# Kernel optimization log

Hardware: AMD Instinct MI355X
Metric: run time of the kernel (lower is better)

Reference implementation:

```python
import jax, jax.numpy as jnp
import numpy as np

B, L, D, H, F, NL, K, G = 2, 2048, 768, 12, 3072, 12, 128, 16
HD = D // H
SCALE = HD ** -0.5


def setup_inputs() -> dict:
    key = jax.random.key(0)
    ks = jax.random.split(key, 8)
    n = lambda k, s, std=0.02: jax.random.normal(k, s, dtype=jnp.float32) * std
    return {
        "x": jax.random.normal(ks[0], (B, L, D), dtype=jnp.float32),
        "pos_conv_w": n(ks[1], (D, D // G, K)),
        "pos_conv_b": jnp.zeros((D,), jnp.float32),
        "ln0_g": jnp.ones((D,), jnp.float32), "ln0_b": jnp.zeros((D,), jnp.float32),
        "Wq": n(ks[2], (NL, D, D)), "bq": jnp.zeros((NL, D), jnp.float32),
        "Wk": n(ks[3], (NL, D, D)), "bk": jnp.zeros((NL, D), jnp.float32),
        "Wv": n(ks[4], (NL, D, D)), "bv": jnp.zeros((NL, D), jnp.float32),
        "Wo": n(ks[5], (NL, D, D)), "bo": jnp.zeros((NL, D), jnp.float32),
        "ln1_g": jnp.ones((NL, D), jnp.float32), "ln1_b": jnp.zeros((NL, D), jnp.float32),
        "W1": n(ks[6], (NL, D, F)), "b1": jnp.zeros((NL, F), jnp.float32),
        "W2": n(ks[7], (NL, F, D)), "b2": jnp.zeros((NL, D), jnp.float32),
        "ln2_g": jnp.ones((NL, D), jnp.float32), "ln2_b": jnp.zeros((NL, D), jnp.float32),
    }


def _ln(x, g, b, eps=1e-5):
    m = jnp.mean(x, axis=-1, keepdims=True)
    v = jnp.mean(jnp.square(x - m), axis=-1, keepdims=True)
    return (x - m) * jax.lax.rsqrt(v + eps) * g + b


def reference(x, pos_conv_w, pos_conv_b, ln0_g, ln0_b, Wq, bq, Wk, bk, Wv, bv, Wo, bo,
              ln1_g, ln1_b, W1, b1, W2, b2, ln2_g, ln2_b):
    b_, l_, d_ = x.shape
    # positional grouped conv embedding (kernel even -> drop last frame), GELU, residual add
    pos = jax.lax.conv_general_dilated(x.transpose(0, 2, 1), pos_conv_w, (1,), [(K // 2, K // 2)],
                                       feature_group_count=G)  # (B, D, L+1)
    pos = pos[:, :, :l_] + pos_conv_b[None, :, None]
    h = x + jax.nn.gelu(pos, approximate=False).transpose(0, 2, 1)
    # post-norm encoder (layer_norm_first=False): LN applied before the layer stack
    h = _ln(h, ln0_g, ln0_b)

    def layer(h, p):
        wq, bq_, wk, bk_, wv, bv_, wo, bo_, g1, be1, w1, bf1, w2, bf2, g2, be2 = p
        r = h
        q = (h @ wq + bq_).reshape(b_, l_, H, HD)
        k = (h @ wk + bk_).reshape(b_, l_, H, HD)
        v = (h @ wv + bv_).reshape(b_, l_, H, HD)
        w = jax.nn.softmax(SCALE * jnp.einsum('blhd,bmhd->bhlm', q, k), axis=-1)
        o = jnp.einsum('bhlm,bmhd->blhd', w, v).reshape(b_, l_, d_)
        h = r + (o @ wo + bo_)
        h = _ln(h, g1, be1)
        ff = jax.nn.gelu(h @ w1 + bf1, approximate=False) @ w2 + bf2
        h = _ln(h + ff, g2, be2)
        return h, None

    h, _ = jax.lax.scan(layer, h, (Wq, bq, Wk, bk, Wv, bv, Wo, bo,
                                   ln1_g, ln1_b, W1, b1, W2, b2, ln2_g, ln2_b))
    return h
```

## Files before the change

kernel.cpp:

```cpp
#include <hip/hip_runtime.h>
#include <hip/hip_bf16.h>
#include <stdint.h>

#define B_ 2
#define L_ 2048
#define D_ 768
#define H_ 12
#define F_ 3072
#define NL_ 12
#define K_ 128
#define G_ 16
#define HD_ 64
#define CPG_ 48
#define M_TOK (B_*L_)
#define SCALE_ 0.125f

typedef __hip_bfloat16 bf16;
typedef __bf16 bf16x8 __attribute__((ext_vector_type(8)));
typedef float f32x4 __attribute__((ext_vector_type(4)));

__device__ __forceinline__ void gload16(const void* g, void* l) {
  __builtin_amdgcn_global_load_lds((const __attribute__((address_space(1))) void*)g,
                                   (__attribute__((address_space(3))) void*)l, 16, 0, 0);
}

__global__ __launch_bounds__(256) void convw_kernel(const float* __restrict__ w,
                                                    bf16* __restrict__ wT2) {
  int idx = blockIdx.x * 256 + threadIdx.x;
  int ci = idx & 63;
  int row = idx >> 6;
  int d = row % 48;
  int t2 = row / 48;
  int kk = t2 & 127;
  int g = t2 >> 7;
  float v = (ci < 48) ? w[(((size_t)(g * 48 + d) * 48) + ci) * 128 + kk] : 0.f;
  wT2[idx] = __float2bfloat16(v);
}

__global__ __launch_bounds__(256) void conv_mfma(const float* __restrict__ x,
                                                 const bf16* __restrict__ wT2,
                                                 const float* __restrict__ bias,
                                                 float* __restrict__ out) {
  const int l0 = blockIdx.x * 64, g = blockIdx.y, b = blockIdx.z;
  const int tid = threadIdx.x, w = tid >> 6, lane = tid & 63;
  const int c15 = lane & 15, g4 = lane >> 4;
  __shared__ __align__(16) bf16 win[192 * 72];
  __shared__ __align__(16) bf16 Wl[2 * 48 * 64];

  if (tid < 192) {
    int lg = l0 - 64 + tid;
    char* dst = (char*)win + tid * 144;
    uint4 z4 = {0u, 0u, 0u, 0u};
    if ((unsigned)lg < 2048u) {
      const float* srow = x + ((size_t)(b * 2048 + lg) * 768 + g * 48);
#pragma unroll
      for (int c = 0; c < 6; ++c) {
        float4 v0 = *(const float4*)(srow + c * 8);
        float4 v1 = *(const float4*)(srow + c * 8 + 4);
        union { bf16 h[8]; uint4 u; } uu;
        uu.h[0] = __float2bfloat16(v0.x); uu.h[1] = __float2bfloat16(v0.y);
        uu.h[2] = __float2bfloat16(v0.z); uu.h[3] = __float2bfloat16(v0.w);
        uu.h[4] = __float2bfloat16(v1.x); uu.h[5] = __float2bfloat16(v1.y);
        uu.h[6] = __float2bfloat16(v1.z); uu.h[7] = __float2bfloat16(v1.w);
        *(uint4*)(dst + c * 16) = uu.u;
      }
    } else {
#pragma unroll
      for (int c = 0; c < 6; ++c) *(uint4*)(dst + c * 16) = z4;
    }
    *(uint4*)(dst + 96) = z4;
    *(uint4*)(dst + 112) = z4;
  }
  __syncthreads();

  f32x4 acc[3];
  const f32x4 vzero = {0.f, 0.f, 0.f, 0.f};
  acc[0] = vzero; acc[1] = vzero; acc[2] = vzero;

  const char* wbase = (const char*)wT2 + (size_t)g * 128 * 48 * 128;

  for (int kp = 0; kp < 64; ++kp) {
#pragma unroll
    for (int i = 0; i < 3; ++i) {
      int coff = w * 3072 + i * 1024;
      int c = coff + (lane << 4);
      int row96 = c >> 7;
      int s = row96 / 48;
      int d = row96 - s * 48;
      int cb2 = c & 127;
      gload16(wbase + ((size_t)((2 * kp + s) * 48 + d)) * 128 + (cb2 ^ ((d & 7) << 4)),
              (char*)Wl + coff);
    }
    __syncthreads();
#pragma unroll
    for (int s = 0; s < 2; ++s) {
      int kk = 2 * kp + s;
#pragma unroll
      for (int cb = 0; cb < 2; ++cb) {
        bf16x8 a = *(const bf16x8*)((const char*)win + (w * 16 + c15 + kk) * 144 + cb * 64 + g4 * 16);
#pragma unroll
        for (int ct = 0; ct < 3; ++ct) {
          int d = ct * 16 + c15;
          bf16x8 bfrag = *(const bf16x8*)((const char*)Wl + s * 6144 + d * 128 +
                                          ((cb * 64 + g4 * 16) ^ ((d & 7) << 4)));
          acc[ct] = __builtin_amdgcn_mfma_f32_16x16x32_bf16(a, bfrag, acc[ct], 0, 0, 0);
        }
      }
    }
    __syncthreads();
  }

#pragma unroll
  for (int ct = 0; ct < 3; ++ct) {
    int dg = g * 48 + ct * 16 + c15;
    float bv = bias[dg];
#pragma unroll
    for (int r = 0; r < 4; ++r) {
      int l = l0 + w * 16 + g4 * 4 + r;
      size_t idx = (size_t)(b * 2048 + l) * 768 + dg;
      float vv = acc[ct][r] + bv;
      vv = 0.5f * vv * (1.0f + erff(vv * 0.70710678f));
      out[idx] = x[idx] + vv;
    }
  }
}

__global__ __launch_bounds__(256) void ln_kernel(const float* __restrict__ a,
                                                 const float* __restrict__ r,
                                                 const float* __restrict__ g,
                                                 const float* __restrict__ be,
                                                 float* __restrict__ out,
                                                 bf16* __restrict__ outb) {
  int w = threadIdx.x >> 6, lane = threadIdx.x & 63;
  size_t row = (size_t)blockIdx.x * 4 + w;
  const float* ar = a + row * 768;
  const float* rr = r ? r + row * 768 : nullptr;
  float4 v[3];
  float s = 0.f;
#pragma unroll
  for (int i = 0; i < 3; ++i) {
    int c = lane * 4 + i * 256;
    float4 vv = *(const float4*)(ar + c);
    if (rr) {
      float4 rv = *(const float4*)(rr + c);
      vv.x += rv.x; vv.y += rv.y; vv.z += rv.z; vv.w += rv.w;
    }
    v[i] = vv;
    s += vv.x + vv.y + vv.z + vv.w;
  }
#pragma unroll
  for (int st = 1; st < 64; st <<= 1) s += __shfl_xor(s, st);
  float mean = s * (1.0f / 768.0f);
  float s2 = 0.f;
#pragma unroll
  for (int i = 0; i < 3; ++i) {
    float dx = v[i].x - mean, dy = v[i].y - mean, dz = v[i].z - mean, dw = v[i].w - mean;
    s2 += dx * dx + dy * dy + dz * dz + dw * dw;
  }
#pragma unroll
  for (int st = 1; st < 64; st <<= 1) s2 += __shfl_xor(s2, st);
  float rstd = rsqrtf(s2 * (1.0f / 768.0f) + 1e-5f);
#pragma unroll
  for (int i = 0; i < 3; ++i) {
    int c = lane * 4 + i * 256;
    float4 gv = *(const float4*)(g + c);
    float4 bv = *(const float4*)(be + c);
    float4 ov;
    ov.x = (v[i].x - mean) * rstd * gv.x + bv.x;
    ov.y = (v[i].y - mean) * rstd * gv.y + bv.y;
    ov.z = (v[i].z - mean) * rstd * gv.z + bv.z;
    ov.w = (v[i].w - mean) * rstd * gv.w + bv.w;
    *(float4*)(out + row * 768 + c) = ov;
    if (outb) {
      union { bf16 h[4]; uint2 u; } pk;
      pk.h[0] = __float2bfloat16(ov.x); pk.h[1] = __float2bfloat16(ov.y);
      pk.h[2] = __float2bfloat16(ov.z); pk.h[3] = __float2bfloat16(ov.w);
      *(uint2*)(outb + row * 768 + c) = pk.u;
    }
  }
}

__global__ __launch_bounds__(256) void castT_kernel(const float* __restrict__ src,
                                                    bf16* __restrict__ dst, int R, int C) {
  __shared__ float t[32][33];
  int c0 = blockIdx.x * 32, r0 = blockIdx.y * 32;
  int tx = threadIdx.x & 31, ty = threadIdx.x >> 5;
#pragma unroll
  for (int i = 0; i < 32; i += 8)
    t[ty + i][tx] = src[(size_t)(r0 + ty + i) * C + (c0 + tx)];
  __syncthreads();
#pragma unroll
  for (int i = 0; i < 32; i += 8)
    dst[(size_t)(c0 + ty + i) * R + (r0 + tx)] = __float2bfloat16(t[tx][ty + i]);
}

__global__ __launch_bounds__(256) void castT_qkv_kernel(const float* __restrict__ q,
                                                        const float* __restrict__ k,
                                                        const float* __restrict__ v,
                                                        bf16* __restrict__ dst) {
  int n0 = blockIdx.x * 32, k0 = blockIdx.y * 32;
  const float* src = (n0 < 768) ? q : (n0 < 1536) ? k : v;
  int nn = (n0 >= 1536) ? (n0 - 1536) : (n0 >= 768 ? n0 - 768 : n0);
  __shared__ float t[32][33];
  int tx = threadIdx.x & 31, ty = threadIdx.x >> 5;
#pragma unroll
  for (int i = 0; i < 32; i += 8)
    t[ty + i][tx] = src[(size_t)(k0 + ty + i) * 768 + nn + tx];
  __syncthreads();
#pragma unroll
  for (int i = 0; i < 32; i += 8)
    dst[(size_t)(n0 + ty + i) * 768 + k0 + tx] = __float2bfloat16(t[tx][ty + i]);
}

__global__ __launch_bounds__(256) void bcat_kernel(const float* __restrict__ bq,
                                                   const float* __restrict__ bk,
                                                   const float* __restrict__ bv,
                                                   float* __restrict__ dst) {
  int i = blockIdx.x * 256 + threadIdx.x;
  if (i >= 2304) return;
  dst[i] = (i < 768) ? bq[i] : (i < 1536) ? bk[i - 768] : bv[i - 1536];
}

__global__ __launch_bounds__(256) void vtrans_kernel(const bf16* __restrict__ qkv,
                                                     bf16* __restrict__ vT) {
  int l0 = blockIdx.x * 32, d0 = blockIdx.y * 32, bh = blockIdx.z;
  int b = bh / 12, h = bh % 12;
  __shared__ bf16 t[32][33];
  int tx = threadIdx.x & 31, ty = threadIdx.x >> 5;
#pragma unroll
  for (int i = 0; i < 32; i += 8)
    t[ty + i][tx] = qkv[(size_t)(b * 2048 + l0 + ty + i) * 2304 + 1536 + h * 64 + d0 + tx];
  __syncthreads();
#pragma unroll
  for (int i = 0; i < 32; i += 8)
    vT[((size_t)bh * 64 + d0 + ty + i) * 2048 + l0 + tx] = t[tx][ty + i];
}

template <int BM, int BN, int GELU, int BF16OUT>
__global__ __launch_bounds__(256) void gemm_bf16(const bf16* __restrict__ A,
                                                 const bf16* __restrict__ BT,
                                                 const float* __restrict__ bias,
                                                 void* __restrict__ Cout,
                                                 int N, int Kd) {
  constexpr int WM = BM / 2, MF = WM / 16;
  constexpr int WN = BN / 2, FN = WN / 16;
  __shared__ bf16 As[BM * 64];
  __shared__ bf16 Bs[BN * 64];
  const int tid = threadIdx.x, w = tid >> 6, lane = tid & 63;
  int gx = gridDim.x;
  int flat = blockIdx.x + gx * blockIdx.y;
  int cpx = (gx * gridDim.y) >> 3;
  int sw = (flat & 7) * cpx + (flat >> 3);
  const int bn = sw % gx, bm = sw / gx;
  const int wr = w >> 1, wc = w & 1;
  const int c15 = lane & 15, g4 = lane >> 4;
  const int lrow8 = lane >> 3;
  const int cb = (lane & 7) * 16;

  f32x4 acc[MF][FN];
  const f32x4 vzero = {0.f, 0.f, 0.f, 0.f};
#pragma unroll
  for (int i = 0; i < MF; ++i)
#pragma unroll
    for (int j = 0; j < FN; ++j) acc[i][j] = vzero;

  const char* Ab = (const char*)A;
  const char* Bb = (const char*)BT;

  for (int k0 = 0; k0 < Kd; k0 += 64) {
#pragma unroll
    for (int i = 0; i < BM / 32; ++i) {
      int t = w + 4 * i;
      int row = t * 8 + lrow8;
      gload16(Ab + ((size_t)(bm * BM + row) * Kd + k0) * 2 + (cb ^ ((row & 7) << 4)),
              (char*)As + t * 1024);
    }
#pragma unroll
    for (int i = 0; i < BN / 32; ++i) {
      int t = w + 4 * i;
      int row = t * 8 + lrow8;
      gload16(Bb + ((size_t)(bn * BN + row) * Kd + k0) * 2 + (cb ^ ((row & 7) << 4)),
              (char*)Bs + t * 1024);
    }
    __syncthreads();
    bf16x8 af[MF][2], bfr[FN][2];
#pragma unroll
    for (int kf = 0; kf < 2; ++kf) {
      int kbyte = kf * 64 + g4 * 16;
#pragma unroll
      for (int mf = 0; mf < MF; ++mf) {
        int row = wr * WM + mf * 16 + c15;
        af[mf][kf] = *(const bf16x8*)((const char*)As + row * 128 + (kbyte ^ ((row & 7) << 4)));
      }
#pragma unroll
      for (int fn = 0; fn < FN; ++fn) {
        int row = wc * WN + fn * 16 + c15;
        bfr[fn][kf] = *(const bf16x8*)((const char*)Bs + row * 128 + (kbyte ^ ((row & 7) << 4)));
      }
    }
    __builtin_amdgcn_s_setprio(1);
#pragma unroll
    for (int mf = 0; mf < MF; ++mf)
#pragma unroll
      for (int fn = 0; fn < FN; ++fn) {
        acc[mf][fn] = __builtin_amdgcn_mfma_f32_16x16x32_bf16(af[mf][0], bfr[fn][0], acc[mf][fn], 0, 0, 0);
        acc[mf][fn] = __builtin_amdgcn_mfma_f32_16x16x32_bf16(af[mf][1], bfr[fn][1], acc[mf][fn], 0, 0, 0);
      }
    __builtin_amdgcn_s_setprio(0);
    __syncthreads();
  }
#pragma unroll
  for (int fn = 0; fn < FN; ++fn) {
    int col = bn * BN + wc * WN + fn * 16 + c15;
    float bv = bias[col];
#pragma unroll
    for (int mf = 0; mf < MF; ++mf) {
#pragma unroll
      for (int r = 0; r < 4; ++r) {
        int row = bm * BM + wr * WM + mf * 16 + g4 * 4 + r;
        float vv = acc[mf][fn][r] + bv;
        if (GELU) vv = 0.5f * vv * (1.0f + erff(vv * 0.70710678f));
        if (BF16OUT) ((bf16*)Cout)[(size_t)row * N + col] = __float2bfloat16(vv);
        else        ((float*)Cout)[(size_t)row * N + col] = vv;
      }
    }
  }
}

__global__ __launch_bounds__(256) void attn_mfma(const bf16* __restrict__ qkv,
                                                 const bf16* __restrict__ vT,
                                                 bf16* __restrict__ ob) {
  int bid = blockIdx.x + 32 * (blockIdx.y + 12 * blockIdx.z);
  int wgid = (bid & 7) * 96 + (bid >> 3);
  const int q0 = (wgid & 31) * 64;
  int bh = wgid >> 5;
  const int h = bh % 12, b = bh / 12;

  const int tid = threadIdx.x, w = tid >> 6, lane = tid & 63;
  const int c15 = lane & 15, g4 = lane >> 4;
  const int lrow8 = lane >> 3;
  const int cb = (lane & 7) * 16;
  __shared__ bf16 Kl[2][4096];
  __shared__ bf16 Vl[2][4096];
  __shared__ bf16 Pl[4096];

  const f32x4 vzero = {0.f, 0.f, 0.f, 0.f};
  const char* qp = (const char*)qkv + (((size_t)(b * 2048 + q0 + w * 16 + c15)) * 2304 + h * 64) * 2;
  bf16x8 qa0 = *(const bf16x8*)(qp + g4 * 16);
  bf16x8 qa1 = *(const bf16x8*)(qp + 64 + g4 * 16);

  bf16x8 b_one;
#pragma unroll
  for (int i = 0; i < 8; ++i) b_one[i] = (__bf16)1.0f;

  f32x4 o[4], o5;
#pragma unroll
  for (int i = 0; i < 4; ++i) o[i] = vzero;
  o5 = vzero;
  float m = -1e30f;
  const float SC2 = 0.18033688f;
  const float THR = 11.54f;

  const char* kgb = (const char*)qkv + (((size_t)(b * 2048)) * 2304 + 768 + h * 64) * 2;
  const char* vgb = (const char*)vT + ((size_t)((b * 12 + h) * 64) * 2048) * 2;
  char* Plw = (char*)Pl + w * 2048;

#define STAGE(kt, bufi)                                                                     \
  {                                                                                         \
    char* Kd = (char*)Kl[bufi];                                                             \
    char* Vd = (char*)Vl[bufi];                                                             \
    _Pragma("unroll")                                                                       \
    for (int i = 0; i < 2; ++i) {                                                           \
      int t = w + 4 * i;                                                                    \
      int rr = t * 8 + lrow8;                                                               \
      gload16(kgb + (size_t)((kt) * 64 + rr) * 4608 + (cb ^ ((rr & 7) << 4)), Kd + t * 1024);\
      gload16(vgb + (size_t)rr * 4096 + (size_t)(kt) * 128 + (cb ^ ((rr & 7) << 4)), Vd + t * 1024);\
    }                                                                                       \
  }

  STAGE(0, 0);
  __syncthreads();

  for (int kt = 0; kt < 32; ++kt) {
    int cur = kt & 1;
    if (kt + 1 < 32) STAGE(kt + 1, cur ^ 1);

    const char* Kc = (const char*)Kl[cur];
    const char* Vc = (const char*)Vl[cur];

    f32x4 sc[4];
    __builtin_amdgcn_s_setprio(1);
#pragma unroll
    for (int fn = 0; fn < 4; ++fn) {
      int key = fn * 16 + c15;
      const char* kr = Kc + key * 128;
      int sw = (key & 7) << 4;
      bf16x8 kb0 = *(const bf16x8*)(kr + ((g4 * 16) ^ sw));
      bf16x8 kb1 = *(const bf16x8*)(kr + ((64 + g4 * 16) ^ sw));
      f32x4 s = __builtin_amdgcn_mfma_f32_16x16x32_bf16(kb0, qa0, vzero, 0, 0, 0);
      s = __builtin_amdgcn_mfma_f32_16x16x32_bf16(kb1, qa1, s, 0, 0, 0);
      sc[fn] = s;
    }
    __builtin_amdgcn_s_setprio(0);

    float pm = fmaxf(
        fmaxf(fmaxf(fmaxf(sc[0][0], sc[0][1]), fmaxf(sc[0][2], sc[0][3])),
              fmaxf(fmaxf(sc[1][0], sc[1][1]), fmaxf(sc[1][2], sc[1][3]))),
        fmaxf(fmaxf(fmaxf(sc[2][0], sc[2][1]), fmaxf(sc[2][2], sc[2][3])),
              fmaxf(fmaxf(sc[3][0], sc[3][1]), fmaxf(sc[3][2], sc[3][3]))));
    int ok = (pm * SC2 <= m + THR) ? 1 : 0;

    if (!__all(ok)) {
      float tm = pm;
      tm = fmaxf(tm, __shfl_xor(tm, 16));
      tm = fmaxf(tm, __shfl_xor(tm, 32));
      float mn = fmaxf(m, tm * SC2);
      float alpha = exp2f(m - mn);
      m = mn;
#pragma unroll
      for (int r = 0; r < 4; ++r) {
        float ar = __shfl(alpha, g4 * 4 + r);
        o[0][r] *= ar; o[1][r] *= ar; o[2][r] *= ar; o[3][r] *= ar;
        o5[r] *= ar;
      }
    }

    {
      char* prow = Plw + c15 * 128;
      int swp = (c15 & 7) << 4;
#pragma unroll
      for (int fn = 0; fn < 4; ++fn) {
        union { bf16 hh[4]; uint2 u; } pk;
#pragma unroll
        for (int r = 0; r < 4; ++r)
          pk.hh[r] = __float2bfloat16(exp2f(fmaf(sc[fn][r], SC2, -m)));
        *(uint2*)(prow + ((fn * 32 + g4 * 8) ^ swp)) = pk.u;
      }
    }

    {
      const char* pr = Plw + c15 * 128;
      int sw = (c15 & 7) << 4;
      bf16x8 pa0 = *(const bf16x8*)(pr + ((g4 * 16) ^ sw));
      bf16x8 pa1 = *(const bf16x8*)(pr + ((64 + g4 * 16) ^ sw));
      __builtin_amdgcn_s_setprio(1);
#pragma unroll
      for (int fh = 0; fh < 4; ++fh) {
        int hd = fh * 16 + c15;
        const char* vr = Vc + hd * 128;
        int swv = (hd & 7) << 4;
        bf16x8 vb0 = *(const bf16x8*)(vr + ((g4 * 16) ^ swv));
        bf16x8 vb1 = *(const bf16x8*)(vr + ((64 + g4 * 16) ^ swv));
        o[fh] = __builtin_amdgcn_mfma_f32_16x16x32_bf16(pa0, vb0, o[fh], 0, 0, 0);
        o[fh] = __builtin_amdgcn_mfma_f32_16x16x32_bf16(pa1, vb1, o[fh], 0, 0, 0);
      }
      o5 = __builtin_amdgcn_mfma_f32_16x16x32_bf16(pa0, b_one, o5, 0, 0, 0);
      o5 = __builtin_amdgcn_mfma_f32_16x16x32_bf16(pa1, b_one, o5, 0, 0, 0);
      __builtin_amdgcn_s_setprio(0);
    }
    __syncthreads();
  }
#undef STAGE

#pragma unroll
  for (int r = 0; r < 4; ++r) {
    float inv = 1.0f / o5[r];
    size_t row = (size_t)(b * 2048 + q0 + w * 16 + g4 * 4 + r);
#pragma unroll
    for (int fh = 0; fh < 4; ++fh)
      ob[row * 768 + h * 64 + fh * 16 + c15] = __float2bfloat16(o[fh][r] * inv);
  }
}

extern "C" void kernel_launch(void* const* d_in, const int* in_sizes, int n_in,
                              void* d_out, int out_size, void* d_ws, size_t ws_size,
                              hipStream_t stream) {
  const float* x      = (const float*)d_in[0];
  const float* pcw    = (const float*)d_in[1];
  const float* pcb    = (const float*)d_in[2];
  const float* ln0_g  = (const float*)d_in[3];
  const float* ln0_b  = (const float*)d_in[4];
  const float* Wq     = (const float*)d_in[5];
  const float* bq     = (const float*)d_in[6];
  const float* Wk     = (const float*)d_in[7];
  const float* bk     = (const float*)d_in[8];
  const float* Wv     = (const float*)d_in[9];
  const float* bv     = (const float*)d_in[10];
  const float* Wo     = (const float*)d_in[11];
  const float* bo     = (const float*)d_in[12];
  const float* ln1_g  = (const float*)d_in[13];
  const float* ln1_b  = (const float*)d_in[14];
  const float* W1     = (const float*)d_in[15];
  const float* b1     = (const float*)d_in[16];
  const float* W2     = (const float*)d_in[17];
  const float* b2     = (const float*)d_in[18];
  const float* ln2_g  = (const float*)d_in[19];
  const float* ln2_b  = (const float*)d_in[20];

  const size_t MDB = (size_t)M_TOK * D_ * 4;
  char* W = (char*)d_ws;
  float* h    = (float*)W;
  float* tmp  = (float*)(W + MDB);
  char*  big  = W + 2 * MDB;
  bf16*  qkv  = (bf16*)big;
  bf16*  ff   = (bf16*)big;
  bf16*  wT2  = (bf16*)big;
  char* p = W + 2 * MDB + 25165824;
  bf16* h_bf  = (bf16*)p; p += (size_t)M_TOK * D_ * 2;
  bf16* obuf  = (bf16*)p; p += (size_t)M_TOK * D_ * 2;
  bf16* vT    = (bf16*)p; p += (size_t)M_TOK * D_ * 2;
  bf16* wqkvb = (bf16*)p; p += (size_t)2304 * 768 * 2;
  bf16* wob   = (bf16*)p; p += (size_t)768 * 768 * 2;
  bf16* w1b   = (bf16*)p; p += (size_t)3072 * 768 * 2;
  bf16* w2b   = (bf16*)p; p += (size_t)768 * 3072 * 2;
  float* bqkv = (float*)p;

  convw_kernel<<<24576, 256, 0, stream>>>(pcw, wT2);
  conv_mfma<<<dim3(32, 16, 2), 256, 0, stream>>>(x, wT2, pcb, tmp);
  ln_kernel<<<M_TOK / 4, 256, 0, stream>>>(tmp, nullptr, ln0_g, ln0_b, h, h_bf);

  for (int l = 0; l < NL_; ++l) {
    const float* wq = Wq + (size_t)l * D_ * D_;
    const float* wk = Wk + (size_t)l * D_ * D_;
    const float* wv = Wv + (size_t)l * D_ * D_;
    const float* wo = Wo + (size_t)l * D_ * D_;
    const float* w1 = W1 + (size_t)l * D_ * F_;
    const float* w2 = W2 + (size_t)l * F_ * D_;

    castT_qkv_kernel<<<dim3(72, 24), 256, 0, stream>>>(wq, wk, wv, wqkvb);
    bcat_kernel<<<9, 256, 0, stream>>>(bq + (size_t)l * D_, bk + (size_t)l * D_, bv + (size_t)l * D_, bqkv);
    castT_kernel<<<dim3(24, 24), 256, 0, stream>>>(wo, wob, 768, 768);
    castT_kernel<<<dim3(96, 24), 256, 0, stream>>>(w1, w1b, 768, 3072);
    castT_kernel<<<dim3(24, 96), 256, 0, stream>>>(w2, w2b, 3072, 768);

    gemm_bf16<128, 128, 0, 1><<<dim3(18, 32), 256, 0, stream>>>(h_bf, wqkvb, bqkv, qkv, 2304, 768);
    vtrans_kernel<<<dim3(64, 2, 24), 256, 0, stream>>>(qkv, vT);
    attn_mfma<<<dim3(32, 12, 2), 256, 0, stream>>>(qkv, vT, obuf);
    gemm_bf16<64, 64, 0, 0><<<dim3(12, 64), 256, 0, stream>>>(obuf, wob, bo + (size_t)l * D_, tmp, 768, 768);
    ln_kernel<<<M_TOK / 4, 256, 0, stream>>>(tmp, h, ln1_g + (size_t)l * D_, ln1_b + (size_t)l * D_, h, h_bf);
    gemm_bf16<128, 128, 1, 1><<<dim3(24, 32), 256, 0, stream>>>(h_bf, w1b, b1 + (size_t)l * F_, ff, 3072, 768);
    gemm_bf16<64, 64, 0, 0><<<dim3(12, 64), 256, 0, stream>>>(ff, w2b, b2 + (size_t)l * D_, tmp, 768, 3072);
    float* out_ln2 = (l == NL_ - 1) ? (float*)d_out : h;
    ln_kernel<<<M_TOK / 4, 256, 0, stream>>>(tmp, h, ln2_g + (size_t)l * D_, ln2_b + (size_t)l * D_, out_ln2, h_bf);
  }
}
```

Before: 2.390 ms.

## Fuse weight prep kernels, write V transposed from QKV GEMM, retile conv

Merges the per-layer weight cast/transpose and bias concat launches into a single prep_weights kernel. The QKV GEMM epilogue now writes V directly in transposed layout, which removes the separate vtrans kernel. The positional conv now computes 128 positions per block instead of 64, uses a swizzled LDS input window and a remapped flat grid, which doubles reuse of each weight tile. The transposed V stores from the GEMM epilogue are strided and uncoalesced, so that write path may cost more than the pass it replaces.

```diff
diff --git a/kernel.cpp b/kernel.cpp
--- a/kernel.cpp
+++ b/kernel.cpp
@@ -41,15 +41,22 @@
                                                  const bf16* __restrict__ wT2,
                                                  const float* __restrict__ bias,
                                                  float* __restrict__ out) {
-  const int l0 = blockIdx.x * 64, g = blockIdx.y, b = blockIdx.z;
+  int flat = blockIdx.x;
+  int wgid = (flat & 7) * 64 + (flat >> 3);
+  const int g = wgid >> 5;
+  int rem = wgid & 31;
+  const int l0 = (rem & 15) * 128;
+  const int b = rem >> 4;
+
   const int tid = threadIdx.x, w = tid >> 6, lane = tid & 63;
   const int c15 = lane & 15, g4 = lane >> 4;
-  __shared__ __align__(16) bf16 win[192 * 72];
+  __shared__ __align__(16) bf16 win[256 * 64];
   __shared__ __align__(16) bf16 Wl[2 * 48 * 64];
 
-  if (tid < 192) {
+  {
     int lg = l0 - 64 + tid;
-    char* dst = (char*)win + tid * 144;
+    char* dst = (char*)win + tid * 128;
+    int swr = (tid & 7) << 4;
     uint4 z4 = {0u, 0u, 0u, 0u};
     if ((unsigned)lg < 2048u) {
       const float* srow = x + ((size_t)(b * 2048 + lg) * 768 + g * 48);
@@ -62,20 +69,23 @@
         uu.h[2] = __float2bfloat16(v0.z); uu.h[3] = __float2bfloat16(v0.w);
         uu.h[4] = __float2bfloat16(v1.x); uu.h[5] = __float2bfloat16(v1.y);
         uu.h[6] = __float2bfloat16(v1.z); uu.h[7] = __float2bfloat16(v1.w);
-        *(uint4*)(dst + c * 16) = uu.u;
+        *(uint4*)(dst + ((c * 16) ^ swr)) = uu.u;
       }
     } else {
 #pragma unroll
-      for (int c = 0; c < 6; ++c) *(uint4*)(dst + c * 16) = z4;
-    }
-    *(uint4*)(dst + 96) = z4;
-    *(uint4*)(dst + 112) = z4;
+      for (int c = 0; c < 6; ++c) *(uint4*)(dst + ((c * 16) ^ swr)) = z4;
+    }
+    *(uint4*)(dst + (96 ^ swr)) = z4;
+    *(uint4*)(dst + (112 ^ swr)) = z4;
   }
   __syncthreads();
 
-  f32x4 acc[3];
+  f32x4 acc[2][3];
   const f32x4 vzero = {0.f, 0.f, 0.f, 0.f};
-  acc[0] = vzero; acc[1] = vzero; acc[2] = vzero;
+#pragma unroll
+  for (int i = 0; i < 2; ++i)
+#pragma unroll
+    for (int j = 0; j < 3; ++j) acc[i][j] = vzero;
 
   const char* wbase = (const char*)wT2 + (size_t)g * 128 * 48 * 128;
 
@@ -97,13 +107,17 @@
       int kk = 2 * kp + s;
 #pragma unroll
       for (int cb = 0; cb < 2; ++cb) {
-        bf16x8 a = *(const bf16x8*)((const char*)win + (w * 16 + c15 + kk) * 144 + cb * 64 + g4 * 16);
+        int a0r = w * 16 + c15 + kk;
+        int a1r = 64 + a0r;
+        bf16x8 a0 = *(const bf16x8*)((const char*)win + a0r * 128 + ((cb * 64 + g4 * 16) ^ ((a0r & 7) << 4)));
+        bf16x8 a1 = *(const bf16x8*)((const char*)win + a1r * 128 + ((cb * 64 + g4 * 16) ^ ((a1r & 7) << 4)));
 #pragma unroll
         for (int ct = 0; ct < 3; ++ct) {
           int d = ct * 16 + c15;
           bf16x8 bfrag = *(const bf16x8*)((const char*)Wl + s * 6144 + d * 128 +
                                           ((cb * 64 + g4 * 16) ^ ((d & 7) << 4)));
-          acc[ct] = __builtin_amdgcn_mfma_f32_16x16x32_bf16(a, bfrag, acc[ct], 0, 0, 0);
+          acc[0][ct] = __builtin_amdgcn_mfma_f32_16x16x32_bf16(a0, bfrag, acc[0][ct], 0, 0, 0);
+          acc[1][ct] = __builtin_amdgcn_mfma_f32_16x16x32_bf16(a1, bfrag, acc[1][ct], 0, 0, 0);
         }
       }
     }
@@ -111,18 +125,20 @@
   }
 
 #pragma unroll
-  for (int ct = 0; ct < 3; ++ct) {
-    int dg = g * 48 + ct * 16 + c15;
-    float bv = bias[dg];
-#pragma unroll
-    for (int r = 0; r < 4; ++r) {
-      int l = l0 + w * 16 + g4 * 4 + r;
-      size_t idx = (size_t)(b * 2048 + l) * 768 + dg;
-      float vv = acc[ct][r] + bv;
-      vv = 0.5f * vv * (1.0f + erff(vv * 0.70710678f));
-      out[idx] = x[idx] + vv;
-    }
-  }
+  for (int ls = 0; ls < 2; ++ls)
+#pragma unroll
+    for (int ct = 0; ct < 3; ++ct) {
+      int dg = g * 48 + ct * 16 + c15;
+      float bv = bias[dg];
+#pragma unroll
+      for (int r = 0; r < 4; ++r) {
+        int l = l0 + ls * 64 + w * 16 + g4 * 4 + r;
+        size_t idx = (size_t)(b * 2048 + l) * 768 + dg;
+        float vv = acc[ls][ct][r] + bv;
+        vv = 0.5f * vv * (1.0f + erff(vv * 0.70710678f));
+        out[idx] = x[idx] + vv;
+      }
+    }
 }
 
 __global__ __launch_bounds__(256) void ln_kernel(const float* __restrict__ a,
@@ -180,68 +196,82 @@
   }
 }
 
-__global__ __launch_bounds__(256) void castT_kernel(const float* __restrict__ src,
-                                                    bf16* __restrict__ dst, int R, int C) {
+__global__ __launch_bounds__(256) void prep_weights(const float* __restrict__ wq,
+                                                    const float* __restrict__ wk,
+                                                    const float* __restrict__ wv,
+                                                    const float* __restrict__ wo,
+                                                    const float* __restrict__ w1,
+                                                    const float* __restrict__ w2,
+                                                    const float* __restrict__ bq_,
+                                                    const float* __restrict__ bk_,
+                                                    const float* __restrict__ bv_,
+                                                    bf16* __restrict__ wqkvb,
+                                                    bf16* __restrict__ wob,
+                                                    bf16* __restrict__ w1b,
+                                                    bf16* __restrict__ w2b,
+                                                    float* __restrict__ bqkv) {
   __shared__ float t[32][33];
-  int c0 = blockIdx.x * 32, r0 = blockIdx.y * 32;
-  int tx = threadIdx.x & 31, ty = threadIdx.x >> 5;
-#pragma unroll
-  for (int i = 0; i < 32; i += 8)
-    t[ty + i][tx] = src[(size_t)(r0 + ty + i) * C + (c0 + tx)];
-  __syncthreads();
-#pragma unroll
-  for (int i = 0; i < 32; i += 8)
-    dst[(size_t)(c0 + ty + i) * R + (r0 + tx)] = __float2bfloat16(t[tx][ty + i]);
-}
-
-__global__ __launch_bounds__(256) void castT_qkv_kernel(const float* __restrict__ q,
-                                                        const float* __restrict__ k,
-                                                        const float* __restrict__ v,
-                                                        bf16* __restrict__ dst) {
-  int n0 = blockIdx.x * 32, k0 = blockIdx.y * 32;
-  const float* src = (n0 < 768) ? q : (n0 < 1536) ? k : v;
-  int nn = (n0 >= 1536) ? (n0 - 1536) : (n0 >= 768 ? n0 - 768 : n0);
-  __shared__ float t[32][33];
-  int tx = threadIdx.x & 31, ty = threadIdx.x >> 5;
-#pragma unroll
-  for (int i = 0; i < 32; i += 8)
-    t[ty + i][tx] = src[(size_t)(k0 + ty + i) * 768 + nn + tx];
-  __syncthreads();
-#pragma unroll
-  for (int i = 0; i < 32; i += 8)
-    dst[(size_t)(n0 + ty + i) * 768 + k0 + tx] = __float2bfloat16(t[tx][ty + i]);
-}
-
-__global__ __launch_bounds__(256) void bcat_kernel(const float* __restrict__ bq,
-                                                   const float* __restrict__ bk,
-                                                   const float* __restrict__ bv,
-                                                   float* __restrict__ dst) {
-  int i = blockIdx.x * 256 + threadIdx.x;
-  if (i >= 2304) return;
-  dst[i] = (i < 768) ? bq[i] : (i < 1536) ? bk[i - 768] : bv[i - 1536];
-}
-
-__global__ __launch_bounds__(256) void vtrans_kernel(const bf16* __restrict__ qkv,
-                                                     bf16* __restrict__ vT) {
-  int l0 = blockIdx.x * 32, d0 = blockIdx.y * 32, bh = blockIdx.z;
-  int b = bh / 12, h = bh % 12;
-  __shared__ bf16 t[32][33];
-  int tx = threadIdx.x & 31, ty = threadIdx.x >> 5;
-#pragma unroll
-  for (int i = 0; i < 32; i += 8)
-    t[ty + i][tx] = qkv[(size_t)(b * 2048 + l0 + ty + i) * 2304 + 1536 + h * 64 + d0 + tx];
-  __syncthreads();
-#pragma unroll
-  for (int i = 0; i < 32; i += 8)
-    vT[((size_t)bh * 64 + d0 + ty + i) * 2048 + l0 + tx] = t[tx][ty + i];
-}
-
-template <int BM, int BN, int GELU, int BF16OUT>
+  int tid = threadIdx.x;
+  int tx = tid & 31, ty = tid >> 5;
+  int blk = blockIdx.x;
+  if (blk >= 6912) {
+    int i = (blk - 6912) * 256 + tid;
+    if (i < 2304) bqkv[i] = (i < 768) ? bq_[i] : (i < 1536) ? bk_[i - 768] : bv_[i - 1536];
+    return;
+  }
+  if (blk < 1728) {
+    int n0 = (blk % 72) * 32, k0 = (blk / 72) * 32;
+    const float* src = (n0 < 768) ? wq : (n0 < 1536) ? wk : wv;
+    int nn = (n0 >= 1536) ? (n0 - 1536) : (n0 >= 768 ? n0 - 768 : n0);
+#pragma unroll
+    for (int i = 0; i < 32; i += 8) t[ty + i][tx] = src[(size_t)(k0 + ty + i) * 768 + nn + tx];
+    __syncthreads();
+#pragma unroll
+    for (int i = 0; i < 32; i += 8)
+      wqkvb[(size_t)(n0 + ty + i) * 768 + k0 + tx] = __float2bfloat16(t[tx][ty + i]);
+    return;
+  }
+  blk -= 1728;
+  if (blk < 576) {
+    int c0 = (blk % 24) * 32, r0 = (blk / 24) * 32;
+#pragma unroll
+    for (int i = 0; i < 32; i += 8) t[ty + i][tx] = wo[(size_t)(r0 + ty + i) * 768 + c0 + tx];
+    __syncthreads();
+#pragma unroll
+    for (int i = 0; i < 32; i += 8)
+      wob[(size_t)(c0 + ty + i) * 768 + r0 + tx] = __float2bfloat16(t[tx][ty + i]);
+    return;
+  }
+  blk -= 576;
+  if (blk < 2304) {
+    int c0 = (blk % 96) * 32, r0 = (blk / 96) * 32;
+#pragma unroll
+    for (int i = 0; i < 32; i += 8) t[ty + i][tx] = w1[(size_t)(r0 + ty + i) * 3072 + c0 + tx];
+    __syncthreads();
+#pragma unroll
+    for (int i = 0; i < 32; i += 8)
+      w1b[(size_t)(c0 + ty + i) * 768 + r0 + tx] = __float2bfloat16(t[tx][ty + i]);
+    return;
+  }
+  blk -= 2304;
+  {
+    int c0 = (blk % 24) * 32, r0 = (blk / 24) * 32;
+#pragma unroll
+    for (int i = 0; i < 32; i += 8) t[ty + i][tx] = w2[(size_t)(r0 + ty + i) * 768 + c0 + tx];
+    __syncthreads();
+#pragma unroll
+    for (int i = 0; i < 32; i += 8)
+      w2b[(size_t)(c0 + ty + i) * 3072 + r0 + tx] = __float2bfloat16(t[tx][ty + i]);
+  }
+}
+
+template <int BM, int BN, int GELU, int BF16OUT, int VOUT = 0>
 __global__ __launch_bounds__(256) void gemm_bf16(const bf16* __restrict__ A,
                                                  const bf16* __restrict__ BT,
                                                  const float* __restrict__ bias,
                                                  void* __restrict__ Cout,
-                                                 int N, int Kd) {
+                                                 int N, int Kd,
+                                                 bf16* __restrict__ vTout = nullptr) {
   constexpr int WM = BM / 2, MF = WM / 16;
   constexpr int WN = BN / 2, FN = WN / 16;
   __shared__ bf16 As[BM * 64];
@@ -320,8 +350,17 @@
         int row = bm * BM + wr * WM + mf * 16 + g4 * 4 + r;
         float vv = acc[mf][fn][r] + bv;
         if (GELU) vv = 0.5f * vv * (1.0f + erff(vv * 0.70710678f));
-        if (BF16OUT) ((bf16*)Cout)[(size_t)row * N + col] = __float2bfloat16(vv);
-        else        ((float*)Cout)[(size_t)row * N + col] = vv;
+        if (BF16OUT) {
+          if (VOUT && col >= 1536) {
+            int hd2 = col - 1536, hh = hd2 >> 6, dd = hd2 & 63;
+            int bb = row >> 11, ll = row & 2047;
+            vTout[((size_t)((bb * 12 + hh) * 64 + dd) << 11) + ll] = __float2bfloat16(vv);
+          } else {
+            ((bf16*)Cout)[(size_t)row * N + col] = __float2bfloat16(vv);
+          }
+        } else {
+          ((float*)Cout)[(size_t)row * N + col] = vv;
+        }
       }
     }
   }
@@ -516,7 +555,7 @@
   float* bqkv = (float*)p;
 
   convw_kernel<<<24576, 256, 0, stream>>>(pcw, wT2);
-  conv_mfma<<<dim3(32, 16, 2), 256, 0, stream>>>(x, wT2, pcb, tmp);
+  conv_mfma<<<512, 256, 0, stream>>>(x, wT2, pcb, tmp);
   ln_kernel<<<M_TOK / 4, 256, 0, stream>>>(tmp, nullptr, ln0_g, ln0_b, h, h_bf);
 
   for (int l = 0; l < NL_; ++l) {
@@ -527,14 +566,11 @@
     const float* w1 = W1 + (size_t)l * D_ * F_;
     const float* w2 = W2 + (size_t)l * F_ * D_;
 
-    castT_qkv_kernel<<<dim3(72, 24), 256, 0, stream>>>(wq, wk, wv, wqkvb);
-    bcat_kernel<<<9, 256, 0, stream>>>(bq + (size_t)l * D_, bk + (size_t)l * D_, bv + (size_t)l * D_, bqkv);
-    castT_kernel<<<dim3(24, 24), 256, 0, stream>>>(wo, wob, 768, 768);
-    castT_kernel<<<dim3(96, 24), 256, 0, stream>>>(w1, w1b, 768, 3072);
-    castT_kernel<<<dim3(24, 96), 256, 0, stream>>>(w2, w2b, 3072, 768);
-
-    gemm_bf16<128, 128, 0, 1><<<dim3(18, 32), 256, 0, stream>>>(h_bf, wqkvb, bqkv, qkv, 2304, 768);
-    vtrans_kernel<<<dim3(64, 2, 24), 256, 0, stream>>>(qkv, vT);
+    prep_weights<<<6921, 256, 0, stream>>>(wq, wk, wv, wo, w1, w2,
+                                           bq + (size_t)l * D_, bk + (size_t)l * D_, bv + (size_t)l * D_,
+                                           wqkvb, wob, w1b, w2b, bqkv);
+
+    gemm_bf16<128, 128, 0, 1, 1><<<dim3(18, 32), 256, 0, stream>>>(h_bf, wqkvb, bqkv, qkv, 2304, 768, vT);
     attn_mfma<<<dim3(32, 12, 2), 256, 0, stream>>>(qkv, vT, obuf);
     gemm_bf16<64, 64, 0, 0><<<dim3(12, 64), 256, 0, stream>>>(obuf, wob, bo + (size_t)l * D_, tmp, 768, 768);
     ln_kernel<<<M_TOK / 4, 256, 0, stream>>>(tmp, h, ln1_g + (size_t)l * D_, ln1_b + (size_t)l * D_, h, h_bf);
```

Result: no change. 2.403 ms (+0.5%).
